# Optimization experiments

Measured on AMD Instinct MI355X. Metric: run time of the kernel, lower is better.

Reference implementation:

```python
import jax, jax.numpy as jnp
import numpy as np

SEQ, EMB, QKV = 4096, 1024, 1024

def setup_inputs() -> dict:
    key = jax.random.key(0)
    k_x, k_q, k_k, k_v = jax.random.split(key, 4)
    scale = 1.0 / np.sqrt(EMB)
    return {
        "x": jax.random.normal(k_x, (SEQ, EMB), dtype=jnp.float32),
        "W_q": jax.random.normal(k_q, (EMB, QKV), dtype=jnp.float32) * scale,
        "W_k": jax.random.normal(k_k, (EMB, QKV), dtype=jnp.float32) * scale,
        "W_v": jax.random.normal(k_v, (EMB, QKV), dtype=jnp.float32) * scale,
    }

def reference(x, W_q, W_k, W_v):
    # Single-head scaled dot-product attention, unbatched: x [S, E]
    d_k = W_q.shape[1]
    Q = x @ W_q          # [S, D]
    K = x @ W_k          # [S, D]
    V = x @ W_v          # [S, D]
    scores = (Q @ K.T) * (1.0 / jnp.sqrt(jnp.asarray(d_k, dtype=x.dtype)))  # [S, S]
    attn = jax.nn.softmax(scores, axis=-1)
    return attn @ V      # [S, D]
```

## Files before the change

kernel.cpp:

```cpp
#include <hip/hip_runtime.h>
#include <cstdint>

#define S_DIM 4096
#define E_DIM 1024
#define D_DIM 1024

typedef __bf16 bf16x8 __attribute__((ext_vector_type(8)));
typedef float  f32x4  __attribute__((ext_vector_type(4)));
typedef unsigned short u16x8 __attribute__((ext_vector_type(8)));
typedef unsigned short u16x4 __attribute__((ext_vector_type(4)));

__device__ __forceinline__ unsigned short f2bf(float f) {
  unsigned u = __float_as_uint(f);
  unsigned r = (u + 0x7fffu + ((u >> 16) & 1u)) >> 16;
  return (unsigned short)r;
}

__device__ __forceinline__ void lds_copy16(const unsigned short* g, const unsigned short* l) {
  auto gp = reinterpret_cast<__attribute__((address_space(1))) unsigned int*>(
      reinterpret_cast<uintptr_t>(g));
  auto lp = reinterpret_cast<__attribute__((address_space(3))) unsigned int*>(
      reinterpret_cast<uintptr_t>(l));
  __builtin_amdgcn_global_load_lds(gp, lp, 16, 0, 0);
}

__global__ __launch_bounds__(256) void prep_kernel(
    const float* __restrict__ x,
    const float* __restrict__ Wq, const float* __restrict__ Wk, const float* __restrict__ Wv,
    unsigned short* __restrict__ xbf, unsigned short* __restrict__ Wt,
    float* __restrict__ lsum) {
  const int z = blockIdx.z;
  const int tid = threadIdx.x;
  if (z < 3) {
    const float* W = (z == 0) ? Wq : (z == 1 ? Wk : Wv);
    unsigned short* out = Wt + (size_t)z * E_DIM * D_DIM;
    __shared__ unsigned short tile[32][33];
    int bc = blockIdx.x * 32, br = blockIdx.y * 32;
    int tx = tid & 31, ty = tid >> 5;
#pragma unroll
    for (int i = 0; i < 32; i += 8)
      tile[ty + i][tx] = f2bf(W[(size_t)(br + ty + i) * D_DIM + bc + tx]);
    __syncthreads();
#pragma unroll
    for (int i = 0; i < 32; i += 8)
      out[(size_t)(bc + ty + i) * E_DIM + br + tx] = tile[tx][ty + i];
  } else {
    int bid = blockIdx.y * 32 + blockIdx.x;
    int i = (bid * 256 + tid) * 16;
#pragma unroll
    for (int h = 0; h < 2; h++) {
      float4 a = *(const float4*)(x + i + h * 8);
      float4 b = *(const float4*)(x + i + h * 8 + 4);
      u16x8 o;
      o[0] = f2bf(a.x); o[1] = f2bf(a.y); o[2] = f2bf(a.z); o[3] = f2bf(a.w);
      o[4] = f2bf(b.x); o[5] = f2bf(b.y); o[6] = f2bf(b.z); o[7] = f2bf(b.w);
      *(u16x8*)(xbf + i + h * 8) = o;
    }
    if (bid < 16) lsum[bid * 256 + tid] = 0.f;
  }
}

template <int MODE, bool SPLIT3, int NBUF>
__global__ __launch_bounds__(256, 2) void gemm_bt_kernel(
    const unsigned short* __restrict__ A, int lda,
    const unsigned short* __restrict__ Bt, int ldb,
    void* __restrict__ Cp, unsigned short* __restrict__ C1,
    unsigned short* __restrict__ C2, int ldc,
    int Kper, float scale, float* __restrict__ lsum) {
  __shared__ __align__(16) unsigned short sA[NBUF][128 * 32];
  __shared__ __align__(16) unsigned short sB[NBUF][128 * 32];

  const int tid = threadIdx.x;

  int flat = blockIdx.y * gridDim.x + blockIdx.x;
  int numInG = 8 * gridDim.x;
  int g = flat / numInG;
  int r = flat - g * numInG;
  const int bm = (g * 8 + (r & 7)) * 128;
  const int bn = (r >> 3) * 128;

  const int wave = tid >> 6;
  const int lane = tid & 63;
  const int q    = lane >> 4;
  const int l16  = lane & 15;
  const int wm   = (wave >> 1) * 64;
  const int wn   = (wave & 1) * 64;

  f32x4 zero = {0.f, 0.f, 0.f, 0.f};
  f32x4 acc[4][4];
#pragma unroll
  for (int t = 0; t < 4; t++)
#pragma unroll
    for (int u = 0; u < 4; u++) acc[t][u] = zero;

  const int srow   = tid >> 2;
  const int schunk = (tid & 3) ^ (srow & 3);
  const unsigned short* ap = A  + (size_t)(bm + srow) * lda + schunk * 8;
  const unsigned short* bp = Bt + (size_t)(bn + srow) * ldb + schunk * 8;
  const int wslot = wave * 512;
  const size_t skipA = (size_t)64 * lda;
  const size_t skipB = (size_t)64 * ldb;

  const int sw = (q ^ (l16 & 3)) * 8;

  auto stage = [&](int koff, int buf) {
    lds_copy16(ap + koff,         sA[buf] + wslot);
    lds_copy16(ap + koff + skipA, sA[buf] + wslot + 2048);
    lds_copy16(bp + koff,         sB[buf] + wslot);
    lds_copy16(bp + koff + skipB, sB[buf] + wslot + 2048);
  };

#pragma unroll
  for (int i = 0; i < NBUF - 1; i++) stage(32 * i, i);

  int cb = 0, db = NBUF - 1;
  for (int k0 = 0; k0 < Kper; k0 += 32) {
    if (k0 + 32 * (NBUF - 1) < Kper) {
      stage(k0 + 32 * (NBUF - 1), db);
      if constexpr (NBUF == 4)
        asm volatile("s_waitcnt vmcnt(12)\n\ts_barrier" ::: "memory");
      else
        asm volatile("s_waitcnt vmcnt(8)\n\ts_barrier" ::: "memory");
    } else {
      const int inflight = ((Kper - k0) >> 5) - 1;
      if (inflight >= 2)      asm volatile("s_waitcnt vmcnt(8)\n\ts_barrier" ::: "memory");
      else if (inflight == 1) asm volatile("s_waitcnt vmcnt(4)\n\ts_barrier" ::: "memory");
      else                    asm volatile("s_waitcnt vmcnt(0)\n\ts_barrier" ::: "memory");
    }

    bf16x8 af[4], bfv[4];
#pragma unroll
    for (int t = 0; t < 4; t++)
      af[t] = *reinterpret_cast<const bf16x8*>(sA[cb] + (wm + t * 16 + l16) * 32 + sw);
#pragma unroll
    for (int u = 0; u < 4; u++)
      bfv[u] = *reinterpret_cast<const bf16x8*>(sB[cb] + (wn + u * 16 + l16) * 32 + sw);
#pragma unroll
    for (int t = 0; t < 4; t++)
#pragma unroll
      for (int u = 0; u < 4; u++)
        acc[t][u] = __builtin_amdgcn_mfma_f32_16x16x32_bf16(af[t], bfv[u], acc[t][u], 0, 0, 0);

    if (k0 + 32 < Kper)
      asm volatile("s_barrier" ::: "memory");
    cb = (cb == NBUF - 1) ? 0 : cb + 1;
    db = (db == NBUF - 1) ? 0 : db + 1;
  }

  unsigned short* cb16 = (unsigned short*)Cp;
  int coloff = bn;
  bool vtrans = false;
  if constexpr (SPLIT3) {
    int which = bn >> 10;
    vtrans = (which == 2);
    cb16 = (which == 0) ? (unsigned short*)Cp : C1;
    coloff = bn & 1023;
  }

  if (SPLIT3 && vtrans) {
#pragma unroll
    for (int t = 0; t < 4; t++) {
#pragma unroll
      for (int u = 0; u < 4; u++) {
        const int row0 = bm + wm + t * 16 + q * 4;
        const int col  = coloff + wn + u * 16 + l16;
        u16x4 pk;
#pragma unroll
        for (int rr = 0; rr < 4; rr++) pk[rr] = f2bf(acc[t][u][rr]);
        *(u16x4*)(C2 + (size_t)col * S_DIM + row0) = pk;
      }
    }
    return;
  }

#pragma unroll
  for (int t = 0; t < 4; t++) {
#pragma unroll
    for (int rr = 0; rr < 4; rr++) {
      const int row = bm + wm + t * 16 + q * 4 + rr;
      float invl = 1.0f;
      if constexpr (MODE == 2) invl = 1.0f / lsum[row];
      float rs = 0.f;
#pragma unroll
      for (int u = 0; u < 4; u++) {
        const int col = coloff + wn + u * 16 + l16;
        float v = acc[t][u][rr] * scale;
        if constexpr (MODE == 0) {
          cb16[(size_t)row * ldc + col] = f2bf(v);
        } else if constexpr (MODE == 1) {
          float p = __expf(v - 8.0f);
          rs += p;
          cb16[(size_t)row * ldc + col] = f2bf(p);
        } else {
          ((float*)Cp)[(size_t)row * ldc + col] = acc[t][u][rr] * invl;
        }
      }
      if constexpr (MODE == 1) {
        rs += __shfl_xor(rs, 1);
        rs += __shfl_xor(rs, 2);
        rs += __shfl_xor(rs, 4);
        rs += __shfl_xor(rs, 8);
        if (l16 == 0) unsafeAtomicAdd(&lsum[row], rs);
      }
    }
  }
}

extern "C" void kernel_launch(void* const* d_in, const int* in_sizes, int n_in,
                              void* d_out, int out_size, void* d_ws, size_t ws_size,
                              hipStream_t stream) {
  const float* x  = (const float*)d_in[0];
  const float* Wq = (const float*)d_in[1];
  const float* Wk = (const float*)d_in[2];
  const float* Wv = (const float*)d_in[3];
  float* out = (float*)d_out;

  char* ws = (char*)d_ws;
  const size_t MB = 1024 * 1024;
  unsigned short* SP   = (unsigned short*)(ws);
  unsigned short* xbf  = (unsigned short*)(ws + 8 * MB);
  unsigned short* Wt   = (unsigned short*)(ws + 16 * MB);
  unsigned short* Qbf  = (unsigned short*)(ws + 32 * MB);
  unsigned short* Kbf  = (unsigned short*)(ws + 40 * MB);
  unsigned short* Vt   = (unsigned short*)(ws + 48 * MB);
  float*          lsum = (float*)(ws + 56 * MB);

  dim3 blk(256);

  dim3 prgrid(32, 32, 4);
  prep_kernel<<<prgrid, blk, 0, stream>>>(x, Wq, Wk, Wv, xbf, Wt, lsum);

  dim3 pgrid(24, 32, 1);
  gemm_bt_kernel<0, true, 3><<<pgrid, blk, 0, stream>>>(
      xbf, E_DIM, Wt, E_DIM, Qbf, Kbf, Vt, D_DIM, E_DIM, 1.0f, nullptr);

  dim3 sgrid(32, 32, 1);
  gemm_bt_kernel<1, false, 3><<<sgrid, blk, 0, stream>>>(
      Qbf, D_DIM, Kbf, D_DIM, SP, nullptr, nullptr, S_DIM, D_DIM, 0.03125f, lsum);

  dim3 ogrid(8, 32, 1);
  gemm_bt_kernel<2, false, 4><<<ogrid, blk, 0, stream>>>(
      SP, S_DIM, Vt, S_DIM, out, nullptr, nullptr, D_DIM, S_DIM, 1.0f, lsum);
}
```

Measured before the change: 228.2 us.

## Add persistent multi-tile loop, split-K for PV GEMM with atomic output

Generalizes the GEMM kernel to process several output tiles per block with a continuous cross-tile prefetch pipeline, and adds split-K via blockIdx.z. The scores GEMM now runs 512 blocks each doing 2 tiles. The PV GEMM splits K in two over 512 blocks, accumulating into a zeroed output with float atomics, and its buffer depth drops from 4 to 3. This is meant to improve occupancy and load balance on the final GEMM and to hide per-tile pipeline ramp, at the cost of an extra memset, atomic output traffic and nondeterministic summation order.

```diff
diff --git a/kernel.cpp b/kernel.cpp
--- a/kernel.cpp
+++ b/kernel.cpp
@@ -66,18 +66,14 @@
     const unsigned short* __restrict__ Bt, int ldb,
     void* __restrict__ Cp, unsigned short* __restrict__ C1,
     unsigned short* __restrict__ C2, int ldc,
-    int Kper, float scale, float* __restrict__ lsum) {
+    int Kper, float scale, float* __restrict__ lsum,
+    int T, int G, int tgx, int itpt_log) {
   __shared__ __align__(16) unsigned short sA[NBUF][128 * 32];
   __shared__ __align__(16) unsigned short sB[NBUF][128 * 32];
 
   const int tid = threadIdx.x;
-
-  int flat = blockIdx.y * gridDim.x + blockIdx.x;
-  int numInG = 8 * gridDim.x;
-  int g = flat / numInG;
-  int r = flat - g * numInG;
-  const int bm = (g * 8 + (r & 7)) * 128;
-  const int bn = (r >> 3) * 128;
+  const int bid = blockIdx.y * gridDim.x + blockIdx.x;
+  const int numInG = 8 * tgx;
 
   const int wave = tid >> 6;
   const int lane = tid & 63;
@@ -86,6 +82,14 @@
   const int wm   = (wave >> 1) * 64;
   const int wn   = (wave & 1) * 64;
 
+  auto tile_bm_bn = [&](int t, int& bm, int& bn) {
+    int f = bid + t * G;
+    int g = f / numInG;
+    int r = f - g * numInG;
+    bm = (g * 8 + (r & 7)) * 128;
+    bn = (r >> 3) * 128;
+  };
+
   f32x4 zero = {0.f, 0.f, 0.f, 0.f};
   f32x4 acc[4][4];
 #pragma unroll
@@ -95,38 +99,107 @@
 
   const int srow   = tid >> 2;
   const int schunk = (tid & 3) ^ (srow & 3);
-  const unsigned short* ap = A  + (size_t)(bm + srow) * lda + schunk * 8;
-  const unsigned short* bp = Bt + (size_t)(bn + srow) * ldb + schunk * 8;
-  const int wslot = wave * 512;
+  const int kbase  = blockIdx.z * Kper;
+  const int wslot  = wave * 512;
   const size_t skipA = (size_t)64 * lda;
   const size_t skipB = (size_t)64 * ldb;
-
   const int sw = (q ^ (l16 & 3)) * 8;
 
-  auto stage = [&](int koff, int buf) {
-    lds_copy16(ap + koff,         sA[buf] + wslot);
-    lds_copy16(ap + koff + skipA, sA[buf] + wslot + 2048);
-    lds_copy16(bp + koff,         sB[buf] + wslot);
-    lds_copy16(bp + koff + skipB, sB[buf] + wslot + 2048);
-  };
-
-#pragma unroll
-  for (int i = 0; i < NBUF - 1; i++) stage(32 * i, i);
-
+  const int itpt  = 1 << itpt_log;
+  const int total = T << itpt_log;
+
+  const unsigned short *sap, *sbp;
+  auto set_stage_tile = [&](int t) {
+    int bm, bn; tile_bm_bn(t, bm, bn);
+    sap = A  + (size_t)(bm + srow) * lda + kbase + schunk * 8;
+    sbp = Bt + (size_t)(bn + srow) * ldb + kbase + schunk * 8;
+  };
+  auto stage = [&](int s, int buf) {
+    const int kk = (s & (itpt - 1)) << 5;
+    lds_copy16(sap + kk,         sA[buf] + wslot);
+    lds_copy16(sap + kk + skipA, sA[buf] + wslot + 2048);
+    lds_copy16(sbp + kk,         sB[buf] + wslot);
+    lds_copy16(sbp + kk + skipB, sB[buf] + wslot + 2048);
+  };
+
+  auto epilogue = [&](int bm, int bn) {
+    unsigned short* cb16 = (unsigned short*)Cp;
+    int coloff = bn;
+    bool vtrans = false;
+    if constexpr (SPLIT3) {
+      int which = bn >> 10;
+      vtrans = (which == 2);
+      cb16 = (which == 0) ? (unsigned short*)Cp : C1;
+      coloff = bn & 1023;
+    }
+    if (SPLIT3 && vtrans) {
+#pragma unroll
+      for (int t = 0; t < 4; t++) {
+#pragma unroll
+        for (int u = 0; u < 4; u++) {
+          const int row0 = bm + wm + t * 16 + q * 4;
+          const int col  = coloff + wn + u * 16 + l16;
+          u16x4 pk;
+#pragma unroll
+          for (int rr = 0; rr < 4; rr++) pk[rr] = f2bf(acc[t][u][rr]);
+          *(u16x4*)(C2 + (size_t)col * S_DIM + row0) = pk;
+        }
+      }
+      return;
+    }
+#pragma unroll
+    for (int t = 0; t < 4; t++) {
+#pragma unroll
+      for (int rr = 0; rr < 4; rr++) {
+        const int row = bm + wm + t * 16 + q * 4 + rr;
+        float invl = 1.0f;
+        if constexpr (MODE == 2) invl = 1.0f / lsum[row];
+        float rs = 0.f;
+#pragma unroll
+        for (int u = 0; u < 4; u++) {
+          const int col = coloff + wn + u * 16 + l16;
+          float v = acc[t][u][rr] * scale;
+          if constexpr (MODE == 0) {
+            cb16[(size_t)row * ldc + col] = f2bf(v);
+          } else if constexpr (MODE == 1) {
+            float p = __expf(v - 8.0f);
+            rs += p;
+            cb16[(size_t)row * ldc + col] = f2bf(p);
+          } else {
+            unsafeAtomicAdd((float*)Cp + (size_t)row * ldc + col, acc[t][u][rr] * invl);
+          }
+        }
+        if constexpr (MODE == 1) {
+          rs += __shfl_xor(rs, 1);
+          rs += __shfl_xor(rs, 2);
+          rs += __shfl_xor(rs, 4);
+          rs += __shfl_xor(rs, 8);
+          if (l16 == 0) unsafeAtomicAdd(&lsum[row], rs);
+        }
+      }
+    }
+  };
+
+  set_stage_tile(0);
+#pragma unroll
+  for (int i = 0; i < NBUF - 1; i++) stage(i, i);
+
+  int c_bm, c_bn;
+  tile_bm_bn(0, c_bm, c_bn);
+  int ctile = 0;
   int cb = 0, db = NBUF - 1;
-  for (int k0 = 0; k0 < Kper; k0 += 32) {
-    if (k0 + 32 * (NBUF - 1) < Kper) {
-      stage(k0 + 32 * (NBUF - 1), db);
-      if constexpr (NBUF == 4)
-        asm volatile("s_waitcnt vmcnt(12)\n\ts_barrier" ::: "memory");
-      else
-        asm volatile("s_waitcnt vmcnt(8)\n\ts_barrier" ::: "memory");
-    } else {
-      const int inflight = ((Kper - k0) >> 5) - 1;
-      if (inflight >= 2)      asm volatile("s_waitcnt vmcnt(8)\n\ts_barrier" ::: "memory");
-      else if (inflight == 1) asm volatile("s_waitcnt vmcnt(4)\n\ts_barrier" ::: "memory");
-      else                    asm volatile("s_waitcnt vmcnt(0)\n\ts_barrier" ::: "memory");
-    }
+
+  for (int i = 0; i < total; i++) {
+    const int s = i + NBUF - 1;
+    if (s < total) {
+      if ((s & (itpt - 1)) == 0) set_stage_tile(s >> itpt_log);
+      stage(s, db);
+    }
+    int ahead = total - 1 - i;
+    if (ahead > NBUF - 1) ahead = NBUF - 1;
+    if (ahead >= 2)      asm volatile("s_waitcnt vmcnt(8)\n\ts_barrier" ::: "memory");
+    else if (ahead == 1) asm volatile("s_waitcnt vmcnt(4)\n\ts_barrier" ::: "memory");
+    else                 asm volatile("s_waitcnt vmcnt(0)\n\ts_barrier" ::: "memory");
 
     bf16x8 af[4], bfv[4];
 #pragma unroll
@@ -141,68 +214,20 @@
       for (int u = 0; u < 4; u++)
         acc[t][u] = __builtin_amdgcn_mfma_f32_16x16x32_bf16(af[t], bfv[u], acc[t][u], 0, 0, 0);
 
-    if (k0 + 32 < Kper)
+    if ((i & (itpt - 1)) == itpt - 1) {
+      epilogue(c_bm, c_bn);
+#pragma unroll
+      for (int t = 0; t < 4; t++)
+#pragma unroll
+        for (int u = 0; u < 4; u++) acc[t][u] = zero;
+      ctile++;
+      if (ctile < T) tile_bm_bn(ctile, c_bm, c_bn);
+    }
+
+    if (i + 1 < total)
       asm volatile("s_barrier" ::: "memory");
     cb = (cb == NBUF - 1) ? 0 : cb + 1;
     db = (db == NBUF - 1) ? 0 : db + 1;
-  }
-
-  unsigned short* cb16 = (unsigned short*)Cp;
-  int coloff = bn;
-  bool vtrans = false;
-  if constexpr (SPLIT3) {
-    int which = bn >> 10;
-    vtrans = (which == 2);
-    cb16 = (which == 0) ? (unsigned short*)Cp : C1;
-    coloff = bn & 1023;
-  }
-
-  if (SPLIT3 && vtrans) {
-#pragma unroll
-    for (int t = 0; t < 4; t++) {
-#pragma unroll
-      for (int u = 0; u < 4; u++) {
-        const int row0 = bm + wm + t * 16 + q * 4;
-        const int col  = coloff + wn + u * 16 + l16;
-        u16x4 pk;
-#pragma unroll
-        for (int rr = 0; rr < 4; rr++) pk[rr] = f2bf(acc[t][u][rr]);
-        *(u16x4*)(C2 + (size_t)col * S_DIM + row0) = pk;
-      }
-    }
-    return;
-  }
-
-#pragma unroll
-  for (int t = 0; t < 4; t++) {
-#pragma unroll
-    for (int rr = 0; rr < 4; rr++) {
-      const int row = bm + wm + t * 16 + q * 4 + rr;
-      float invl = 1.0f;
-      if constexpr (MODE == 2) invl = 1.0f / lsum[row];
-      float rs = 0.f;
-#pragma unroll
-      for (int u = 0; u < 4; u++) {
-        const int col = coloff + wn + u * 16 + l16;
-        float v = acc[t][u][rr] * scale;
-        if constexpr (MODE == 0) {
-          cb16[(size_t)row * ldc + col] = f2bf(v);
-        } else if constexpr (MODE == 1) {
-          float p = __expf(v - 8.0f);
-          rs += p;
-          cb16[(size_t)row * ldc + col] = f2bf(p);
-        } else {
-          ((float*)Cp)[(size_t)row * ldc + col] = acc[t][u][rr] * invl;
-        }
-      }
-      if constexpr (MODE == 1) {
-        rs += __shfl_xor(rs, 1);
-        rs += __shfl_xor(rs, 2);
-        rs += __shfl_xor(rs, 4);
-        rs += __shfl_xor(rs, 8);
-        if (l16 == 0) unsafeAtomicAdd(&lsum[row], rs);
-      }
-    }
   }
 }
 
@@ -232,13 +257,17 @@
 
   dim3 pgrid(24, 32, 1);
   gemm_bt_kernel<0, true, 3><<<pgrid, blk, 0, stream>>>(
-      xbf, E_DIM, Wt, E_DIM, Qbf, Kbf, Vt, D_DIM, E_DIM, 1.0f, nullptr);
-
-  dim3 sgrid(32, 32, 1);
+      xbf, E_DIM, Wt, E_DIM, Qbf, Kbf, Vt, D_DIM, E_DIM, 1.0f, nullptr,
+      1, 768, 24, 5);
+
+  dim3 sgrid(32, 16, 1);
   gemm_bt_kernel<1, false, 3><<<sgrid, blk, 0, stream>>>(
-      Qbf, D_DIM, Kbf, D_DIM, SP, nullptr, nullptr, S_DIM, D_DIM, 0.03125f, lsum);
-
-  dim3 ogrid(8, 32, 1);
-  gemm_bt_kernel<2, false, 4><<<ogrid, blk, 0, stream>>>(
-      SP, S_DIM, Vt, S_DIM, out, nullptr, nullptr, D_DIM, S_DIM, 1.0f, lsum);
-}
+      Qbf, D_DIM, Kbf, D_DIM, SP, nullptr, nullptr, S_DIM, D_DIM, 0.03125f, lsum,
+      2, 512, 32, 5);
+
+  hipMemsetAsync(out, 0, (size_t)S_DIM * D_DIM * sizeof(float), stream);
+  dim3 ogrid(8, 32, 2);
+  gemm_bt_kernel<2, false, 3><<<ogrid, blk, 0, stream>>>(
+      SP, S_DIM, Vt, S_DIM, out, nullptr, nullptr, D_DIM, S_DIM / 2, 1.0f, lsum,
+      1, 256, 8, 6);
+}
```

Result: no change. 231.5 us (+1.4%).
